# Optimization experiments

Hardware: AMD Instinct MI355X
Metric: run time of the kernel (lower is better)

The kernel has to match this reference:

```python
import jax, jax.numpy as jnp
import numpy as np

LN_EPS = 1e-5
L2_EPS = 1e-12
SCALE = 8.0

def setup_inputs() -> dict:
    key = jax.random.key(0)
    k0, k1, k2 = jax.random.split(key, 3)
    b, c, H, W = 16, 256, 64, 64
    heads, dim_head = 8, 32
    dim_inner = heads * dim_head  # 256
    x = jax.random.normal(k0, (b, c, H, W), dtype=jnp.float32)
    ln_gamma = jnp.ones((c,), jnp.float32)
    ln_beta = jnp.zeros((c,), jnp.float32)
    W_qkv = jax.random.normal(k1, (c, 3 * dim_inner), dtype=jnp.float32) * 0.02
    temperature = jnp.ones((heads,), jnp.float32)
    W_out = jax.random.normal(k2, (dim_inner, c), dtype=jnp.float32) * 0.02
    b_out = jnp.zeros((c,), jnp.float32)
    return {"x": x, "ln_gamma": ln_gamma, "ln_beta": ln_beta, "W_qkv": W_qkv,
            "temperature": temperature, "W_out": W_out, "b_out": b_out, "heads": heads}

def _l2norm(t):
    # F.normalize(t, dim=-1): divide by clamped L2 norm along last axis
    n = jnp.sqrt(jnp.sum(t * t, axis=-1, keepdims=True))
    return t / jnp.maximum(n, L2_EPS)

def reference(x, ln_gamma, ln_beta, W_qkv, temperature, W_out, b_out, heads):
    b, c, H, W = x.shape
    n = H * W
    dim_head = W_qkv.shape[1] // (3 * heads)
    # b c h w -> b (h w) c
    t = jnp.transpose(x, (0, 2, 3, 1)).reshape(b, n, c)
    # LayerNorm over channel dim (affine)
    mu = jnp.mean(t, axis=-1, keepdims=True)
    var = jnp.mean(jnp.square(t - mu), axis=-1, keepdims=True)
    t = (t - mu) * jax.lax.rsqrt(var + LN_EPS) * ln_gamma + ln_beta
    # qkv projection; split last dim as (qkv, heads, dim_head) -> (3, b, h, d, n)
    qkv = (t @ W_qkv).reshape(b, n, 3, heads, dim_head)
    qkv = jnp.transpose(qkv, (2, 0, 3, 4, 1))
    q, k, v = qkv[0], qkv[1], qkv[2]
    q = _l2norm(q) * jnp.exp(temperature)[None, :, None, None]
    k = _l2norm(k)
    # cross-covariance attention over channel dim: sim is [b, h, d, d]
    sim = jnp.einsum('bhin,bhjn->bhij', q, k) * SCALE
    attn = jax.nn.softmax(sim, axis=-1)
    out = jnp.einsum('bhij,bhjn->bhin', attn, v)  # [b, h, d, n]
    # b h d n -> b n (h d)
    out = jnp.transpose(out, (0, 3, 1, 2)).reshape(b, n, heads * dim_head)
    out = out @ W_out + b_out
    # b (h w) c -> b c h w
    return jnp.transpose(out.reshape(b, H, W, c), (0, 3, 1, 2))
```

## Files before the change

### kernel.cpp

```cpp
#include <hip/hip_runtime.h>

typedef unsigned short u16;
typedef __bf16 bf16x8 __attribute__((ext_vector_type(8)));
typedef float f32x4 __attribute__((ext_vector_type(4)));

#define MFMA(a, b, c) __builtin_amdgcn_mfma_f32_16x16x32_bf16((a), (b), (c), 0, 0, 0)

__device__ __forceinline__ u16 f2bf(float f) {
    unsigned u = __float_as_uint(f);
    unsigned r = (u + 0x7fffu + ((u >> 16) & 1u)) >> 16;
    return (u16)r;
}
__device__ __forceinline__ float bf2f(u16 h) { return __uint_as_float(((unsigned)h) << 16); }


__global__ __launch_bounds__(256) void k_ln(const float* __restrict__ x,
                                            const float* __restrict__ gamma,
                                            const float* __restrict__ beta,
                                            u16* __restrict__ xlnT) {
    int bid = blockIdx.x;
    int b = bid >> 6, nt = bid & 63;
    int nb = nt * 64;
    __shared__ unsigned xsu[256 * 33];
    __shared__ float muv[64], rsv[64];
    __shared__ float redS[8 * 64], redS2[8 * 64];
    int t = threadIdx.x;
    {
        int np = t & 31;
        int c0 = t >> 5;
        const float* xp = x + ((size_t)b * 256) * 4096 + nb + np * 2;
        for (int i = 0; i < 32; i++) {
            int c = c0 + i * 8;
            float2 f = *(const float2*)(xp + (size_t)c * 4096);
            unsigned u = (unsigned)f2bf(f.x) | ((unsigned)f2bf(f.y) << 16);
            xsu[c * 33 + np] = u;
        }
    }
    __syncthreads();
    {
        int np = t & 31, q = t >> 5;
        float s0 = 0, s20 = 0, s1 = 0, s21 = 0;
        for (int i = 0; i < 32; i++) {
            unsigned u = xsu[(q * 32 + i) * 33 + np];
            float a = bf2f((u16)(u & 0xffffu));
            float bv = bf2f((u16)(u >> 16));
            s0 += a; s20 += a * a; s1 += bv; s21 += bv * bv;
        }
        redS[q * 64 + np * 2] = s0;  redS[q * 64 + np * 2 + 1] = s1;
        redS2[q * 64 + np * 2] = s20; redS2[q * 64 + np * 2 + 1] = s21;
    }
    __syncthreads();
    if (t < 64) {
        float s = 0, s2 = 0;
        for (int q = 0; q < 8; q++) { s += redS[q * 64 + t]; s2 += redS2[q * 64 + t]; }
        float m = s * (1.f / 256.f);
        float var = s2 * (1.f / 256.f) - m * m;
        muv[t] = m;
        rsv[t] = rsqrtf(var + 1e-5f);
    }
    __syncthreads();
    {
        int c4 = (t & 63) * 4;
        int ng = t >> 6;
        float g[4], e[4];
        for (int j = 0; j < 4; j++) { g[j] = gamma[c4 + j]; e[j] = beta[c4 + j]; }
        for (int i = 0; i < 16; i++) {
            int n = ng * 16 + i;
            float m = muv[n], rs = rsv[n];
            u16 h[4];
            for (int j = 0; j < 4; j++) {
                unsigned u = xsu[(c4 + j) * 33 + (n >> 1)];
                u16 raw = (n & 1) ? (u16)(u >> 16) : (u16)(u & 0xffffu);
                float v = (bf2f(raw) - m) * rs * g[j] + e[j];
                h[j] = f2bf(v);
            }
            uint2 w2;
            w2.x = (unsigned)h[0] | ((unsigned)h[1] << 16);
            w2.y = (unsigned)h[2] | ((unsigned)h[3] << 16);
            *(uint2*)(xlnT + ((size_t)(b * 4096 + nb + n)) * 256 + c4) = w2;
        }
    }
}

__global__ __launch_bounds__(256) void k_prep(const float* __restrict__ Wqkv,
                                              const float* __restrict__ Wout,
                                              u16* __restrict__ WqkvT, u16* __restrict__ WoutT,
                                              float* __restrict__ sims) {
    int i = blockIdx.x * 256 + threadIdx.x;
    if (i < 768 * 256) { int o = i >> 8, c = i & 255; WqkvT[i] = f2bf(Wqkv[c * 768 + o]); }
    if (i < 256 * 256) { int o = i >> 8, c = i & 255; WoutT[i] = f2bf(Wout[c * 256 + o]); }
    if (i < 128 * 1024) sims[i] = 0.f;
}

__global__ __launch_bounds__(256) void k_gemm(const u16* __restrict__ A, const u16* __restrict__ Bb,
                                              int mtiles, u16* __restrict__ o16,
                                              float* __restrict__ o32, const float* __restrict__ bias,
                                              int mode) {
    int bid = blockIdx.x;
    int per_b = mtiles * 32;
    int b = bid / per_b;
    int r2 = bid % per_b;
    int mbase = (r2 >> 5) * 128, nbase = (r2 & 31) * 128;
    __shared__ u16 aT[128 * 40];
    __shared__ u16 bT[128 * 40];
    int t = threadIdx.x, w = t >> 6, lane = t & 63, l15 = lane & 15, quad = lane >> 4;
    const u16* Bp = Bb + (size_t)b * 4096 * 256;
    f32x4 acc[2][8];
    f32x4 z = {0.f, 0.f, 0.f, 0.f};
    for (int fm = 0; fm < 2; fm++)
        for (int fn = 0; fn < 8; fn++) acc[fm][fn] = z;
    int arow = t >> 1, ac = (t & 1) * 16;
    for (int kt = 0; kt < 8; kt++) {
        int kb = kt * 32;
        if (kt) __syncthreads();
        {
            const uint4* g = (const uint4*)(A + (size_t)(mbase + arow) * 256 + kb + ac);
            uint4 p0 = g[0], p1 = g[1];
            *(uint4*)&aT[arow * 40 + ac] = p0;
            *(uint4*)&aT[arow * 40 + ac + 8] = p1;
        }
        {
            const uint4* g = (const uint4*)(Bp + (size_t)(nbase + arow) * 256 + kb + ac);
            uint4 p0 = g[0], p1 = g[1];
            *(uint4*)&bT[arow * 40 + ac] = p0;
            *(uint4*)&bT[arow * 40 + ac + 8] = p1;
        }
        __syncthreads();
        bf16x8 af0 = *(const bf16x8*)&aT[(w * 32 + l15) * 40 + quad * 8];
        bf16x8 af1 = *(const bf16x8*)&aT[(w * 32 + 16 + l15) * 40 + quad * 8];
        for (int fn = 0; fn < 8; fn++) {
            bf16x8 bfr = *(const bf16x8*)&bT[(fn * 16 + l15) * 40 + quad * 8];
            acc[0][fn] = MFMA(af0, bfr, acc[0][fn]);
            acc[1][fn] = MFMA(af1, bfr, acc[1][fn]);
        }
    }
    for (int fm = 0; fm < 2; fm++)
        for (int fn = 0; fn < 8; fn++)
            for (int r = 0; r < 4; r++) {
                int row = mbase + w * 32 + fm * 16 + quad * 4 + r;
                int col = nbase + fn * 16 + l15;
                float v = acc[fm][fn][r];
                if (mode == 0)
                    o16[((size_t)b * 768 + row) * 4096 + col] = f2bf(v);
                else
                    o32[((size_t)b * 256 + row) * 4096 + col] = v + bias[row];
            }
}

__global__ __launch_bounds__(256) void k_norms(const u16* __restrict__ qkv, float* __restrict__ normsq) {
    int bid = blockIdx.x;
    int b = bid >> 6, rg = bid & 63;
    int t = threadIdx.x;
    int r8 = t >> 5, l32 = t & 31;
    int o = rg * 8 + r8;
    const u16* p = qkv + ((size_t)b * 768 + o) * 4096 + l32 * 8;
    float s = 0.f;
    for (int i = 0; i < 16; i++) {
        uint4 u = *(const uint4*)(p + i * 256);
        const u16* us = (const u16*)&u;
        for (int jj = 0; jj < 8; jj++) { float f = bf2f(us[jj]); s += f * f; }
    }
    s += __shfl_down(s, 16, 32);
    s += __shfl_down(s, 8, 32);
    s += __shfl_down(s, 4, 32);
    s += __shfl_down(s, 2, 32);
    s += __shfl_down(s, 1, 32);
    if (l32 == 0) normsq[b * 512 + o] = s;
}

__global__ __launch_bounds__(256) void k_sim(const u16* __restrict__ qkv, float* __restrict__ sims) {
    int bid = blockIdx.x;
    int bh = bid >> 1, half = bid & 1;
    int b = bh >> 3, h = bh & 7;
    __shared__ u16 qs[32 * 264];
    __shared__ u16 ks[32 * 264];
    int t = threadIdx.x, w = t >> 6, lane = t & 63, l15 = lane & 15, quad = lane >> 4;
    int ib = w >> 1, jb = w & 1;
    const u16* qbase = qkv + ((size_t)(b * 768) + h * 32) * 4096;
    const u16* kbase = qkv + ((size_t)(b * 768) + 256 + h * 32) * 4096;
    int col8 = t & 31, rb = t >> 5;
    f32x4 acc = {0.f, 0.f, 0.f, 0.f};
    for (int kc = 0; kc < 8; kc++) {
        int kb = half * 2048 + kc * 256;
        __syncthreads();
        for (int i = 0; i < 4; i++) {
            int r = rb + i * 8;
            uint4 pq = *(const uint4*)(qbase + (size_t)r * 4096 + kb + col8 * 8);
            *(uint4*)&qs[r * 264 + col8 * 8] = pq;
            uint4 pk = *(const uint4*)(kbase + (size_t)r * 4096 + kb + col8 * 8);
            *(uint4*)&ks[r * 264 + col8 * 8] = pk;
        }
        __syncthreads();
        for (int s = 0; s < 8; s++) {
            bf16x8 a = *(const bf16x8*)&qs[(ib * 16 + l15) * 264 + s * 32 + quad * 8];
            bf16x8 bb = *(const bf16x8*)&ks[(jb * 16 + l15) * 264 + s * 32 + quad * 8];
            acc = MFMA(a, bb, acc);
        }
    }
    float* sp = sims + (size_t)bh * 1024;
    for (int r = 0; r < 4; r++) {
        int row = ib * 16 + quad * 4 + r, col = jb * 16 + l15;
        atomicAdd(sp + row * 32 + col, acc[r]);
    }
}

__global__ __launch_bounds__(64) void k_soft(const float* __restrict__ sims,
                                             const float* __restrict__ normsq,
                                             const float* __restrict__ temp, u16* __restrict__ attn) {
    int bh = blockIdx.x;
    int b = bh >> 3, h = bh & 7;
    __shared__ float scq[32], sck[32];
    int t = threadIdx.x;
    if (t < 32)
        scq[t] = expf(temp[h]) * 8.0f / fmaxf(sqrtf(normsq[b * 512 + h * 32 + t]), 1e-12f);
    else {
        int d = t - 32;
        sck[d] = 1.0f / fmaxf(sqrtf(normsq[b * 512 + 256 + h * 32 + d]), 1e-12f);
    }
    __syncthreads();
    if (t < 32) {
        float row[32];
        float m = -1e30f;
        const float* sp = sims + (size_t)bh * 1024 + t * 32;
        float sq = scq[t];
        for (int j = 0; j < 32; j++) { float v = sp[j] * sq * sck[j]; row[j] = v; m = fmaxf(m, v); }
        float s = 0.f;
        for (int j = 0; j < 32; j++) { float p = expf(row[j] - m); row[j] = p; s += p; }
        float inv = 1.f / s;
        u16* ap = attn + (size_t)bh * 1024 + t * 32;
        for (int j = 0; j < 32; j++) ap[j] = f2bf(row[j] * inv);
    }
}

__global__ __launch_bounds__(256) void k_pv(const u16* __restrict__ qkv, const u16* __restrict__ attn,
                                            u16* __restrict__ oaT) {
    int bid = blockIdx.x;
    int nc = bid & 15, h = (bid >> 4) & 7, b = bid >> 7;
    int nb = nc * 256;
    __shared__ u16 vt[256 * 40];
    int t = threadIdx.x, w = t >> 6, lane = t & 63, l15 = lane & 15, quad = lane >> 4;
    const u16* ap = attn + (size_t)(b * 8 + h) * 1024;
    bf16x8 a0 = *(const bf16x8*)(ap + l15 * 32 + quad * 8);
    bf16x8 a1 = *(const bf16x8*)(ap + (16 + l15) * 32 + quad * 8);
    const u16* vp = qkv + ((size_t)(b * 768) + 512 + h * 32) * 4096 + nb;
    int col8 = t & 31, rb = t >> 5;
    for (int i = 0; i < 4; i++) {
        int j = rb + i * 8;
        uint4 p = *(const uint4*)(vp + (size_t)j * 4096 + col8 * 8);
        const u16* us = (const u16*)&p;
        int ch = j >> 3;
        for (int jj = 0; jj < 8; jj++) {
            int nl = col8 * 8 + jj;
            vt[nl * 40 + ((ch ^ (col8 & 3)) << 3) + (j & 7)] = us[jj];
        }
    }
    __syncthreads();
    f32x4 z = {0.f, 0.f, 0.f, 0.f};
    for (int mm = 0; mm < 4; mm++) {
        int nlb = (w * 4 + mm) * 16;
        int nl = nlb + l15;
        bf16x8 vf = *(const bf16x8*)&vt[nl * 40 + ((quad ^ ((nl >> 3) & 3)) << 3)];
        f32x4 d0 = MFMA(vf, a0, z);
        f32x4 d1 = MFMA(vf, a1, z);
        for (int r = 0; r < 4; r++) {
            int n = nb + nlb + quad * 4 + r;
            size_t base = ((size_t)(b * 4096) + n) * 256 + h * 32;
            oaT[base + l15] = f2bf(d0[r]);
            oaT[base + 16 + l15] = f2bf(d1[r]);
        }
    }
}

extern "C" void kernel_launch(void* const* d_in, const int* in_sizes, int n_in,
                              void* d_out, int out_size, void* d_ws, size_t ws_size,
                              hipStream_t stream) {
    const float* x     = (const float*)d_in[0];
    const float* gamma = (const float*)d_in[1];
    const float* beta  = (const float*)d_in[2];
    const float* Wqkv  = (const float*)d_in[3];
    const float* temp  = (const float*)d_in[4];
    const float* Wout  = (const float*)d_in[5];
    const float* bout  = (const float*)d_in[6];
    float* out = (float*)d_out;

    char* ws = (char*)d_ws;
    size_t off = 0;
    auto alloc = [&](size_t nbytes) -> void* {
        void* p = ws + off;
        off = (off + nbytes + 255) & ~(size_t)255;
        return p;
    };
    u16* xlnT    = (u16*)alloc((size_t)16 * 4096 * 256 * 2);
    u16* WqkvT   = (u16*)alloc((size_t)768 * 256 * 2);
    u16* WoutT   = (u16*)alloc((size_t)256 * 256 * 2);
    u16* qkv     = (u16*)alloc((size_t)16 * 768 * 4096 * 2);
    float* normsq = (float*)alloc((size_t)16 * 512 * 4);
    float* sims   = (float*)alloc((size_t)128 * 1024 * 4);
    u16* attn    = (u16*)alloc((size_t)128 * 1024 * 2);
    u16* oaT     = (u16*)alloc((size_t)16 * 4096 * 256 * 2);
    (void)ws_size; (void)in_sizes; (void)n_in; (void)out_size;

    hipLaunchKernelGGL(k_ln, dim3(1024), dim3(256), 0, stream, x, gamma, beta, xlnT);
    hipLaunchKernelGGL(k_prep, dim3(768), dim3(256), 0, stream, Wqkv, Wout, WqkvT, WoutT, sims);
    hipLaunchKernelGGL(k_gemm, dim3(3072), dim3(256), 0, stream, WqkvT, xlnT, 6,
                       qkv, (float*)nullptr, (const float*)nullptr, 0);
    hipLaunchKernelGGL(k_norms, dim3(1024), dim3(256), 0, stream, qkv, normsq);
    hipLaunchKernelGGL(k_sim, dim3(256), dim3(256), 0, stream, qkv, sims);
    hipLaunchKernelGGL(k_soft, dim3(128), dim3(64), 0, stream, sims, normsq, temp, attn);
    hipLaunchKernelGGL(k_pv, dim3(2048), dim3(256), 0, stream, qkv, attn, oaT);
    hipLaunchKernelGGL(k_gemm, dim3(1024), dim3(256), 0, stream, WoutT, oaT, 2,
                       (u16*)nullptr, out, bout, 1);
}
```

Baseline: 261.6 us.

## Fold attention into output projection, fuse norms into sim, use LDS-direct loads

Multiplies W_out by the per-head softmax attention matrix to form a per-batch 256x256 matrix, which is applied directly to a transposed V produced by the QKV GEMM. This removes the separate PV kernel and its intermediate write and read. The L2 norm sums are fused into the sim kernel with atomics, and the sim work is split across more blocks. The GEMM now stages tiles through global_load_lds with swizzled LDS layout instead of register round trips. The risks are added rounding from the bf16 fused matrix and extra atomic contention.

After: 231.9 us. -11.4%, faster.

```diff
diff --git a/kernel.cpp b/kernel.cpp
--- a/kernel.cpp
+++ b/kernel.cpp
@@ -12,6 +12,12 @@
     return (u16)r;
 }
 __device__ __forceinline__ float bf2f(u16 h) { return __uint_as_float(((unsigned)h) << 16); }
+
+typedef unsigned int u32_g __attribute__((address_space(1)));
+typedef unsigned int u32_l __attribute__((address_space(3)));
+__device__ __forceinline__ void gload16(const void* g, void* l) {
+    __builtin_amdgcn_global_load_lds((const u32_g*)g, (u32_l*)l, 16, 0, 0);
+}
 
 
 __global__ __launch_bounds__(256) void k_ln(const float* __restrict__ x,
@@ -85,110 +91,125 @@
 __global__ __launch_bounds__(256) void k_prep(const float* __restrict__ Wqkv,
                                               const float* __restrict__ Wout,
                                               u16* __restrict__ WqkvT, u16* __restrict__ WoutT,
-                                              float* __restrict__ sims) {
+                                              float* __restrict__ sims, float* __restrict__ normsq) {
     int i = blockIdx.x * 256 + threadIdx.x;
     if (i < 768 * 256) { int o = i >> 8, c = i & 255; WqkvT[i] = f2bf(Wqkv[c * 768 + o]); }
     if (i < 256 * 256) { int o = i >> 8, c = i & 255; WoutT[i] = f2bf(Wout[c * 256 + o]); }
     if (i < 128 * 1024) sims[i] = 0.f;
-}
-
-__global__ __launch_bounds__(256) void k_gemm(const u16* __restrict__ A, const u16* __restrict__ Bb,
-                                              int mtiles, u16* __restrict__ o16,
+    if (i < 16 * 512) normsq[i] = 0.f;
+}
+
+__global__ __launch_bounds__(256) void k_gemm(const u16* __restrict__ A, size_t aStrB,
+                                              const u16* __restrict__ Bb, size_t bStrB,
+                                              int mtiles, int mrow0,
+                                              u16* __restrict__ o16,
                                               float* __restrict__ o32, const float* __restrict__ bias,
                                               int mode) {
+    extern __shared__ __align__(16) u16 smem[];
+    u16* aT = smem;
+    u16* bT = smem + 128 * 32;
     int bid = blockIdx.x;
     int per_b = mtiles * 32;
     int b = bid / per_b;
     int r2 = bid % per_b;
-    int mbase = (r2 >> 5) * 128, nbase = (r2 & 31) * 128;
-    __shared__ u16 aT[128 * 40];
-    __shared__ u16 bT[128 * 40];
+    int mbase = mrow0 + (r2 >> 5) * 128, nbase = (r2 & 31) * 128;
     int t = threadIdx.x, w = t >> 6, lane = t & 63, l15 = lane & 15, quad = lane >> 4;
-    const u16* Bp = Bb + (size_t)b * 4096 * 256;
+    const u16* Ap = A + (size_t)b * aStrB;
+    const u16* Bp = Bb + (size_t)b * bStrB;
+    int srow = lane >> 2;
+    int g8 = (((lane & 3) ^ ((lane >> 3) & 3)) << 3);
+    const u16* gA = Ap + (size_t)(mbase + w * 32 + srow) * 256 + g8;
+    const u16* gB = Bp + (size_t)(nbase + w * 32 + srow) * 256 + g8;
+    u16* lA = aT + w * 1024;
+    u16* lB = bT + w * 1024;
+    int cOff = ((quad ^ ((l15 >> 1) & 3)) << 3);
     f32x4 acc[2][8];
     f32x4 z = {0.f, 0.f, 0.f, 0.f};
     for (int fm = 0; fm < 2; fm++)
         for (int fn = 0; fn < 8; fn++) acc[fm][fn] = z;
-    int arow = t >> 1, ac = (t & 1) * 16;
     for (int kt = 0; kt < 8; kt++) {
         int kb = kt * 32;
         if (kt) __syncthreads();
-        {
-            const uint4* g = (const uint4*)(A + (size_t)(mbase + arow) * 256 + kb + ac);
-            uint4 p0 = g[0], p1 = g[1];
-            *(uint4*)&aT[arow * 40 + ac] = p0;
-            *(uint4*)&aT[arow * 40 + ac + 8] = p1;
-        }
-        {
-            const uint4* g = (const uint4*)(Bp + (size_t)(nbase + arow) * 256 + kb + ac);
-            uint4 p0 = g[0], p1 = g[1];
-            *(uint4*)&bT[arow * 40 + ac] = p0;
-            *(uint4*)&bT[arow * 40 + ac + 8] = p1;
-        }
+        gload16(gA + kb, lA);
+        gload16(gA + 16 * 256 + kb, lA + 512);
+        gload16(gB + kb, lB);
+        gload16(gB + 16 * 256 + kb, lB + 512);
         __syncthreads();
-        bf16x8 af0 = *(const bf16x8*)&aT[(w * 32 + l15) * 40 + quad * 8];
-        bf16x8 af1 = *(const bf16x8*)&aT[(w * 32 + 16 + l15) * 40 + quad * 8];
+        bf16x8 af0 = *(const bf16x8*)&aT[(w * 32 + l15) * 32 + cOff];
+        bf16x8 af1 = *(const bf16x8*)&aT[(w * 32 + 16 + l15) * 32 + cOff];
         for (int fn = 0; fn < 8; fn++) {
-            bf16x8 bfr = *(const bf16x8*)&bT[(fn * 16 + l15) * 40 + quad * 8];
+            bf16x8 bfr = *(const bf16x8*)&bT[(fn * 16 + l15) * 32 + cOff];
             acc[0][fn] = MFMA(af0, bfr, acc[0][fn]);
             acc[1][fn] = MFMA(af1, bfr, acc[1][fn]);
         }
     }
-    for (int fm = 0; fm < 2; fm++)
-        for (int fn = 0; fn < 8; fn++)
-            for (int r = 0; r < 4; r++) {
-                int row = mbase + w * 32 + fm * 16 + quad * 4 + r;
-                int col = nbase + fn * 16 + l15;
-                float v = acc[fm][fn][r];
-                if (mode == 0)
-                    o16[((size_t)b * 768 + row) * 4096 + col] = f2bf(v);
-                else
-                    o32[((size_t)b * 256 + row) * 4096 + col] = v + bias[row];
+    if (mode == 0) {
+        for (int fm = 0; fm < 2; fm++)
+            for (int fn = 0; fn < 8; fn++)
+                for (int r = 0; r < 4; r++) {
+                    int row = mbase + w * 32 + fm * 16 + quad * 4 + r;
+                    int col = nbase + fn * 16 + l15;
+                    o16[((size_t)b * 512 + row) * 4096 + col] = f2bf(acc[fm][fn][r]);
+                }
+    } else if (mode == 1) {
+        for (int fm = 0; fm < 2; fm++)
+            for (int fn = 0; fn < 8; fn++)
+                for (int r = 0; r < 4; r++) {
+                    int row = mbase + w * 32 + fm * 16 + quad * 4 + r;
+                    int col = nbase + fn * 16 + l15;
+                    o32[((size_t)b * 256 + row) * 4096 + col] = acc[fm][fn][r] + bias[row];
+                }
+    } else {
+        __syncthreads();
+        u16* tp = smem;
+        for (int fm = 0; fm < 2; fm++)
+            for (int fn = 0; fn < 8; fn++) {
+                unsigned p01 = (unsigned)f2bf(acc[fm][fn][0]) | ((unsigned)f2bf(acc[fm][fn][1]) << 16);
+                unsigned p23 = (unsigned)f2bf(acc[fm][fn][2]) | ((unsigned)f2bf(acc[fm][fn][3]) << 16);
+                uint2 pk; pk.x = p01; pk.y = p23;
+                *(uint2*)&tp[(fn * 16 + l15) * 136 + w * 32 + fm * 16 + quad * 4] = pk;
             }
-}
-
-__global__ __launch_bounds__(256) void k_norms(const u16* __restrict__ qkv, float* __restrict__ normsq) {
+        __syncthreads();
+        int jb0 = mbase - 512;
+        for (int p = 0; p < 8; p++) {
+            int col = p * 16 + (t >> 4);
+            int ch = t & 15;
+            uint4 v = *(const uint4*)&tp[col * 136 + ch * 8];
+            *(uint4*)(o16 + ((size_t)b * 4096 + nbase + col) * 256 + jb0 + ch * 8) = v;
+        }
+    }
+}
+
+__global__ __launch_bounds__(256) void k_sim(const u16* __restrict__ qk, float* __restrict__ sims,
+                                             float* __restrict__ normsq) {
     int bid = blockIdx.x;
-    int b = bid >> 6, rg = bid & 63;
-    int t = threadIdx.x;
-    int r8 = t >> 5, l32 = t & 31;
-    int o = rg * 8 + r8;
-    const u16* p = qkv + ((size_t)b * 768 + o) * 4096 + l32 * 8;
-    float s = 0.f;
-    for (int i = 0; i < 16; i++) {
-        uint4 u = *(const uint4*)(p + i * 256);
-        const u16* us = (const u16*)&u;
-        for (int jj = 0; jj < 8; jj++) { float f = bf2f(us[jj]); s += f * f; }
-    }
-    s += __shfl_down(s, 16, 32);
-    s += __shfl_down(s, 8, 32);
-    s += __shfl_down(s, 4, 32);
-    s += __shfl_down(s, 2, 32);
-    s += __shfl_down(s, 1, 32);
-    if (l32 == 0) normsq[b * 512 + o] = s;
-}
-
-__global__ __launch_bounds__(256) void k_sim(const u16* __restrict__ qkv, float* __restrict__ sims) {
-    int bid = blockIdx.x;
-    int bh = bid >> 1, half = bid & 1;
+    int ns = bid & 7, bh = bid >> 3;
     int b = bh >> 3, h = bh & 7;
     __shared__ u16 qs[32 * 264];
     __shared__ u16 ks[32 * 264];
     int t = threadIdx.x, w = t >> 6, lane = t & 63, l15 = lane & 15, quad = lane >> 4;
     int ib = w >> 1, jb = w & 1;
-    const u16* qbase = qkv + ((size_t)(b * 768) + h * 32) * 4096;
-    const u16* kbase = qkv + ((size_t)(b * 768) + 256 + h * 32) * 4096;
+    const u16* qbase = qk + ((size_t)(b * 512) + h * 32) * 4096;
+    const u16* kbase = qk + ((size_t)(b * 512) + 256 + h * 32) * 4096;
     int col8 = t & 31, rb = t >> 5;
     f32x4 acc = {0.f, 0.f, 0.f, 0.f};
-    for (int kc = 0; kc < 8; kc++) {
-        int kb = half * 2048 + kc * 256;
-        __syncthreads();
+    float sq[4] = {0.f, 0.f, 0.f, 0.f}, sk[4] = {0.f, 0.f, 0.f, 0.f};
+    for (int kc = 0; kc < 2; kc++) {
+        int kb = ns * 512 + kc * 256;
+        if (kc) __syncthreads();
+#pragma unroll
         for (int i = 0; i < 4; i++) {
             int r = rb + i * 8;
             uint4 pq = *(const uint4*)(qbase + (size_t)r * 4096 + kb + col8 * 8);
             *(uint4*)&qs[r * 264 + col8 * 8] = pq;
+            const u16* us = (const u16*)&pq;
+#pragma unroll
+            for (int jj = 0; jj < 8; jj++) { float f = bf2f(us[jj]); sq[i] += f * f; }
             uint4 pk = *(const uint4*)(kbase + (size_t)r * 4096 + kb + col8 * 8);
             *(uint4*)&ks[r * 264 + col8 * 8] = pk;
+            const u16* uk = (const u16*)&pk;
+#pragma unroll
+            for (int jj = 0; jj < 8; jj++) { float f = bf2f(uk[jj]); sk[i] += f * f; }
         }
         __syncthreads();
         for (int s = 0; s < 8; s++) {
@@ -197,6 +218,21 @@
             acc = MFMA(a, bb, acc);
         }
     }
+#pragma unroll
+    for (int i = 0; i < 4; i++) {
+#pragma unroll
+        for (int m = 16; m >= 1; m >>= 1) {
+            sq[i] += __shfl_xor(sq[i], m, 32);
+            sk[i] += __shfl_xor(sk[i], m, 32);
+        }
+    }
+    if (col8 == 0) {
+#pragma unroll
+        for (int i = 0; i < 4; i++) {
+            atomicAdd(normsq + b * 512 + h * 32 + rb + i * 8, sq[i]);
+            atomicAdd(normsq + b * 512 + 256 + h * 32 + rb + i * 8, sk[i]);
+        }
+    }
     float* sp = sims + (size_t)bh * 1024;
     for (int r = 0; r < 4; r++) {
         int row = ib * 16 + quad * 4 + r, col = jb * 16 + l15;
@@ -204,16 +240,19 @@
     }
 }
 
-__global__ __launch_bounds__(64) void k_soft(const float* __restrict__ sims,
-                                             const float* __restrict__ normsq,
-                                             const float* __restrict__ temp, u16* __restrict__ attn) {
+__global__ __launch_bounds__(256) void k_softmw(const float* __restrict__ sims,
+                                                const float* __restrict__ normsq,
+                                                const float* __restrict__ temp,
+                                                const u16* __restrict__ WoutT,
+                                                u16* __restrict__ Mb) {
     int bh = blockIdx.x;
     int b = bh >> 3, h = bh & 7;
+    __shared__ float as[32 * 32];
     __shared__ float scq[32], sck[32];
     int t = threadIdx.x;
     if (t < 32)
         scq[t] = expf(temp[h]) * 8.0f / fmaxf(sqrtf(normsq[b * 512 + h * 32 + t]), 1e-12f);
-    else {
+    else if (t < 64) {
         int d = t - 32;
         sck[d] = 1.0f / fmaxf(sqrtf(normsq[b * 512 + 256 + h * 32 + d]), 1e-12f);
     }
@@ -223,51 +262,37 @@
         float m = -1e30f;
         const float* sp = sims + (size_t)bh * 1024 + t * 32;
         float sq = scq[t];
+#pragma unroll
         for (int j = 0; j < 32; j++) { float v = sp[j] * sq * sck[j]; row[j] = v; m = fmaxf(m, v); }
         float s = 0.f;
+#pragma unroll
         for (int j = 0; j < 32; j++) { float p = expf(row[j] - m); row[j] = p; s += p; }
         float inv = 1.f / s;
-        u16* ap = attn + (size_t)bh * 1024 + t * 32;
-        for (int j = 0; j < 32; j++) ap[j] = f2bf(row[j] * inv);
-    }
-}
-
-__global__ __launch_bounds__(256) void k_pv(const u16* __restrict__ qkv, const u16* __restrict__ attn,
-                                            u16* __restrict__ oaT) {
-    int bid = blockIdx.x;
-    int nc = bid & 15, h = (bid >> 4) & 7, b = bid >> 7;
-    int nb = nc * 256;
-    __shared__ u16 vt[256 * 40];
-    int t = threadIdx.x, w = t >> 6, lane = t & 63, l15 = lane & 15, quad = lane >> 4;
-    const u16* ap = attn + (size_t)(b * 8 + h) * 1024;
-    bf16x8 a0 = *(const bf16x8*)(ap + l15 * 32 + quad * 8);
-    bf16x8 a1 = *(const bf16x8*)(ap + (16 + l15) * 32 + quad * 8);
-    const u16* vp = qkv + ((size_t)(b * 768) + 512 + h * 32) * 4096 + nb;
-    int col8 = t & 31, rb = t >> 5;
-    for (int i = 0; i < 4; i++) {
-        int j = rb + i * 8;
-        uint4 p = *(const uint4*)(vp + (size_t)j * 4096 + col8 * 8);
-        const u16* us = (const u16*)&p;
-        int ch = j >> 3;
+#pragma unroll
+        for (int j = 0; j < 32; j++) as[t * 32 + j] = row[j] * inv;
+    }
+    __syncthreads();
+    float wv[32];
+    const u16* wp = WoutT + (size_t)t * 256 + h * 32;
+#pragma unroll
+    for (int d = 0; d < 32; d++) wv[d] = bf2f(wp[d]);
+    u16* mp = Mb + ((size_t)b * 256 + t) * 256 + h * 32;
+    for (int j0 = 0; j0 < 32; j0 += 8) {
+        u16 hh[8];
+#pragma unroll
         for (int jj = 0; jj < 8; jj++) {
-            int nl = col8 * 8 + jj;
-            vt[nl * 40 + ((ch ^ (col8 & 3)) << 3) + (j & 7)] = us[jj];
-        }
-    }
-    __syncthreads();
-    f32x4 z = {0.f, 0.f, 0.f, 0.f};
-    for (int mm = 0; mm < 4; mm++) {
-        int nlb = (w * 4 + mm) * 16;
-        int nl = nlb + l15;
-        bf16x8 vf = *(const bf16x8*)&vt[nl * 40 + ((quad ^ ((nl >> 3) & 3)) << 3)];
-        f32x4 d0 = MFMA(vf, a0, z);
-        f32x4 d1 = MFMA(vf, a1, z);
-        for (int r = 0; r < 4; r++) {
-            int n = nb + nlb + quad * 4 + r;
-            size_t base = ((size_t)(b * 4096) + n) * 256 + h * 32;
-            oaT[base + l15] = f2bf(d0[r]);
-            oaT[base + 16 + l15] = f2bf(d1[r]);
-        }
+            int j = j0 + jj;
+            float s = 0.f;
+#pragma unroll
+            for (int d = 0; d < 32; d++) s += wv[d] * as[d * 32 + j];
+            hh[jj] = f2bf(s);
+        }
+        uint4 pk;
+        pk.x = (unsigned)hh[0] | ((unsigned)hh[1] << 16);
+        pk.y = (unsigned)hh[2] | ((unsigned)hh[3] << 16);
+        pk.z = (unsigned)hh[4] | ((unsigned)hh[5] << 16);
+        pk.w = (unsigned)hh[6] | ((unsigned)hh[7] << 16);
+        *(uint4*)(mp + j0) = pk;
     }
 }
 
@@ -293,21 +318,24 @@
     u16* xlnT    = (u16*)alloc((size_t)16 * 4096 * 256 * 2);
     u16* WqkvT   = (u16*)alloc((size_t)768 * 256 * 2);
     u16* WoutT   = (u16*)alloc((size_t)256 * 256 * 2);
-    u16* qkv     = (u16*)alloc((size_t)16 * 768 * 4096 * 2);
+    u16* qk      = (u16*)alloc((size_t)16 * 512 * 4096 * 2);
+    u16* vT      = (u16*)alloc((size_t)16 * 4096 * 256 * 2);
+    u16* Mb      = (u16*)alloc((size_t)16 * 256 * 256 * 2);
     float* normsq = (float*)alloc((size_t)16 * 512 * 4);
     float* sims   = (float*)alloc((size_t)128 * 1024 * 4);
-    u16* attn    = (u16*)alloc((size_t)128 * 1024 * 2);
-    u16* oaT     = (u16*)alloc((size_t)16 * 4096 * 256 * 2);
     (void)ws_size; (void)in_sizes; (void)n_in; (void)out_size;
 
     hipLaunchKernelGGL(k_ln, dim3(1024), dim3(256), 0, stream, x, gamma, beta, xlnT);
-    hipLaunchKernelGGL(k_prep, dim3(768), dim3(256), 0, stream, Wqkv, Wout, WqkvT, WoutT, sims);
-    hipLaunchKernelGGL(k_gemm, dim3(3072), dim3(256), 0, stream, WqkvT, xlnT, 6,
-                       qkv, (float*)nullptr, (const float*)nullptr, 0);
-    hipLaunchKernelGGL(k_norms, dim3(1024), dim3(256), 0, stream, qkv, normsq);
-    hipLaunchKernelGGL(k_sim, dim3(256), dim3(256), 0, stream, qkv, sims);
-    hipLaunchKernelGGL(k_soft, dim3(128), dim3(64), 0, stream, sims, normsq, temp, attn);
-    hipLaunchKernelGGL(k_pv, dim3(2048), dim3(256), 0, stream, qkv, attn, oaT);
-    hipLaunchKernelGGL(k_gemm, dim3(1024), dim3(256), 0, stream, WoutT, oaT, 2,
+    hipLaunchKernelGGL(k_prep, dim3(768), dim3(256), 0, stream, Wqkv, Wout, WqkvT, WoutT, sims, normsq);
+    hipLaunchKernelGGL(k_gemm, dim3(2048), dim3(256), 16384, stream,
+                       WqkvT, (size_t)0, xlnT, (size_t)4096 * 256, 4, 0,
+                       qk, (float*)nullptr, (const float*)nullptr, 0);
+    hipLaunchKernelGGL(k_gemm, dim3(1024), dim3(256), 34816, stream,
+                       WqkvT, (size_t)0, xlnT, (size_t)4096 * 256, 2, 512,
+                       vT, (float*)nullptr, (const float*)nullptr, 2);
+    hipLaunchKernelGGL(k_sim, dim3(1024), dim3(256), 0, stream, qk, sims, normsq);
+    hipLaunchKernelGGL(k_softmw, dim3(128), dim3(256), 0, stream, sims, normsq, temp, WoutT, Mb);
+    hipLaunchKernelGGL(k_gemm, dim3(1024), dim3(256), 16384, stream,
+                       Mb, (size_t)256 * 256, vT, (size_t)4096 * 256, 2, 0,
                        (u16*)nullptr, out, bout, 1);
 }
```
